# Optimization experiments

Hardware: AMD Instinct MI355X
Metric: run time of the kernel (lower is better)

The kernel has to match this reference:

```python
import jax, jax.numpy as jnp
import numpy as np

EMBED_DIM = 1024
N_HEAD = 16

def setup_inputs() -> dict:
    key = jax.random.key(0)
    ks = jax.random.split(key, 5)
    C = EMBED_DIM
    x = jax.random.normal(ks[0], (2, 2048, C), dtype=jnp.float32)
    s = 1.0 / np.sqrt(C)
    W_attn = jax.random.normal(ks[1], (C, 3 * C), dtype=jnp.float32) * s
    b_attn = jnp.zeros((3 * C,), dtype=jnp.float32)
    W_proj = jax.random.normal(ks[2], (C, C), dtype=jnp.float32) * s
    b_proj = jnp.zeros((C,), dtype=jnp.float32)
    return {"x": x, "W_attn": W_attn, "b_attn": b_attn, "W_proj": W_proj, "b_proj": b_proj}

def reference(x, W_attn, b_attn, W_proj, b_proj):
    B, T, C = x.shape
    H = N_HEAD
    D = C // H
    qkv = x @ W_attn + b_attn                      # [B,T,3C]
    q, k, v = jnp.split(qkv, 3, axis=-1)
    # [B,H,T,D]
    q = q.reshape(B, T, H, D).transpose(0, 2, 1, 3)
    k = k.reshape(B, T, H, D).transpose(0, 2, 1, 3)
    v = v.reshape(B, T, H, D).transpose(0, 2, 1, 3)
    att = jnp.einsum('bhqd,bhkd->bhqk', q, k) * (1.0 / jnp.sqrt(jnp.asarray(D, x.dtype)))
    causal = jnp.tril(jnp.ones((T, T), dtype=bool))
    att = jnp.where(causal, att, -jnp.inf)
    att = jax.nn.softmax(att, axis=-1)
    y = jnp.einsum('bhqk,bhkd->bhqd', att, v)      # [B,H,T,D]
    y = y.transpose(0, 2, 1, 3).reshape(B, T, C)
    return y @ W_proj + b_proj
```

## Files before the change

### kernel.cpp

```cpp
#include <hip/hip_runtime.h>
#include <stdint.h>

typedef __attribute__((ext_vector_type(4))) float f32x4;
typedef __attribute__((ext_vector_type(8))) __bf16 bf16x8;
typedef __attribute__((ext_vector_type(8))) unsigned short u16x8;

__device__ __forceinline__ unsigned short f2b(float f) {
  unsigned u = __float_as_uint(f);
  u += 0x7FFFu + ((u >> 16) & 1u);
  return (unsigned short)(u >> 16);
}
__device__ __forceinline__ float b2f(unsigned short s) {
  unsigned u = (unsigned)s << 16;
  return __uint_as_float(u);
}
__device__ __forceinline__ unsigned cvtpk_bf16(float lo, float hi) {
  unsigned r;
  asm("v_cvt_pk_bf16_f32 %0, %1, %2" : "=v"(r) : "v"(lo), "v"(hi));
  return r;
}

__device__ __forceinline__ void gload_lds16(const void* g, void* l) {
  typedef __attribute__((address_space(1))) void GV1;
  typedef __attribute__((address_space(3))) void LV3;
  __builtin_amdgcn_global_load_lds((GV1*)(void*)g, (LV3*)l, 16, 0, 0);
}

__device__ __forceinline__ void tile_barrier_keep2() {
  asm volatile("s_waitcnt vmcnt(2)" ::: "memory");
  __builtin_amdgcn_sched_barrier(0);
  __builtin_amdgcn_s_barrier();
  __builtin_amdgcn_sched_barrier(0);
}
__device__ __forceinline__ void tile_barrier_keep0() {
  asm volatile("s_waitcnt vmcnt(0)" ::: "memory");
  __builtin_amdgcn_sched_barrier(0);
  __builtin_amdgcn_s_barrier();
  __builtin_amdgcn_sched_barrier(0);
}

__global__ __launch_bounds__(256) void convert_f32_bf16(const float* __restrict__ in,
                                                        unsigned short* __restrict__ out, int n) {
  int i = (blockIdx.x * 256 + threadIdx.x) * 8;
  if (i >= n) return;
  float4 a = *(const float4*)(in + i);
  float4 b = *(const float4*)(in + i + 4);
  u16x8 r;
  r[0] = f2b(a.x); r[1] = f2b(a.y); r[2] = f2b(a.z); r[3] = f2b(a.w);
  r[4] = f2b(b.x); r[5] = f2b(b.y); r[6] = f2b(b.z); r[7] = f2b(b.w);
  *(u16x8*)(out + i) = r;
}

__global__ __launch_bounds__(256) void transpose_f32_bf16(const float* __restrict__ W,
                                                          unsigned short* __restrict__ Wt,
                                                          int K, int N) {
  __shared__ unsigned short tile[32][33];
  int n0 = blockIdx.x * 32, k0 = blockIdx.y * 32;
  int tx = threadIdx.x, ty = threadIdx.y;
  #pragma unroll
  for (int j = 0; j < 32; j += 8)
    tile[ty + j][tx] = f2b(W[(size_t)(k0 + ty + j) * N + n0 + tx]);
  __syncthreads();
  #pragma unroll
  for (int j = 0; j < 32; j += 8)
    Wt[(size_t)(n0 + ty + j) * K + k0 + tx] = tile[tx][ty + j];
}

template <bool OUT_BF16, bool VSPLIT>
__global__ __launch_bounds__(512) void gemm_bt(const unsigned short* __restrict__ A,
                                               const unsigned short* __restrict__ Bt,
                                               const float* __restrict__ bias,
                                               void* __restrict__ Cout,
                                               unsigned short* __restrict__ vT,
                                               int M, int N, int K) {
  __shared__ unsigned short SMEM[32768];
  const int m0 = blockIdx.x * 128, n0 = blockIdx.y * 128;
  const int tid = threadIdx.x;
  const int w = tid >> 6, l = tid & 63;
  const int wm = w >> 2, wn = w & 3;
  const int c = l & 15, g = l >> 4;
  const int NT = K >> 6;
  const unsigned short* aptr[2];
  const unsigned short* bptr[2];
  #pragma unroll
  for (int i = 0; i < 2; ++i) {
    int rb = w * 16 + i * 8;
    aptr[i] = A  + (size_t)(m0 + rb + (l >> 3)) * K + (l & 7) * 8;
    bptr[i] = Bt + (size_t)(n0 + rb + (l >> 3)) * K + (l & 7) * 8;
  }
  f32x4 acc[4][2] = {};
  #pragma unroll
  for (int i = 0; i < 2; ++i) {
    int rb = w * 16 + i * 8;
    gload_lds16(aptr[i], &SMEM[rb * 64]);
    gload_lds16(bptr[i], &SMEM[8192 + rb * 64]);
  }
  __syncthreads();
  for (int t = 0; t < NT; ++t) {
    const int cur = t & 1;
    const unsigned short* Ab = &SMEM[cur * 16384];
    const unsigned short* Bb = &SMEM[cur * 16384 + 8192];
    if (t + 1 < NT) {
      unsigned short* An = &SMEM[(cur ^ 1) * 16384];
      unsigned short* Bn = &SMEM[(cur ^ 1) * 16384 + 8192];
      #pragma unroll
      for (int i = 0; i < 2; ++i) {
        int rb = w * 16 + i * 8;
        gload_lds16(aptr[i] + (size_t)(t + 1) * 64, &An[rb * 64]);
        gload_lds16(bptr[i] + (size_t)(t + 1) * 64, &Bn[rb * 64]);
      }
    }
    #pragma unroll
    for (int ks = 0; ks < 2; ++ks) {
      bf16x8 af[4], bf[2];
      #pragma unroll
      for (int mi = 0; mi < 4; ++mi)
        af[mi] = *(const bf16x8*)&Ab[(wm * 64 + mi * 16 + c) * 64 + ks * 32 + g * 8];
      #pragma unroll
      for (int ni = 0; ni < 2; ++ni)
        bf[ni] = *(const bf16x8*)&Bb[(wn * 32 + ni * 16 + c) * 64 + ks * 32 + g * 8];
      __builtin_amdgcn_s_setprio(1);
      #pragma unroll
      for (int mi = 0; mi < 4; ++mi)
        #pragma unroll
        for (int ni = 0; ni < 2; ++ni)
          acc[mi][ni] = __builtin_amdgcn_mfma_f32_16x16x32_bf16(af[mi], bf[ni], acc[mi][ni], 0, 0, 0);
      __builtin_amdgcn_s_setprio(0);
    }
    __syncthreads();
  }
  if (VSPLIT && n0 >= 2048) {
    unsigned short* TR = SMEM;
    #pragma unroll
    for (int mi = 0; mi < 4; ++mi)
      #pragma unroll
      for (int ni = 0; ni < 2; ++ni) {
        int cl = wn * 32 + ni * 16 + c;
        float bv = bias[n0 + cl];
        int rlb = wm * 64 + mi * 16 + 4 * g;
        ushort4 o4;
        o4.x = f2b(acc[mi][ni][0] + bv); o4.y = f2b(acc[mi][ni][1] + bv);
        o4.z = f2b(acc[mi][ni][2] + bv); o4.w = f2b(acc[mi][ni][3] + bv);
        *(ushort4*)&TR[cl * 136 + rlb] = o4;
      }
    __syncthreads();
    const int d0 = n0 - 2048;
    #pragma unroll
    for (int p = 0; p < 4; ++p) {
      int rowl = p * 32 + (tid >> 4);
      *(u16x8*)(vT + (size_t)(d0 + rowl) * 4096 + m0 + (tid & 15) * 8) =
          *(const u16x8*)&TR[rowl * 136 + (tid & 15) * 8];
    }
    return;
  }
  const int NS = VSPLIT ? 2048 : N;
  #pragma unroll
  for (int mi = 0; mi < 4; ++mi) {
    #pragma unroll
    for (int ni = 0; ni < 2; ++ni) {
      int colg = n0 + wn * 32 + ni * 16 + c;
      float bv = bias[colg];
      #pragma unroll
      for (int r = 0; r < 4; ++r) {
        int rowg = m0 + wm * 64 + mi * 16 + 4 * g + r;
        float v = acc[mi][ni][r] + bv;
        if (OUT_BF16)
          ((unsigned short*)Cout)[(size_t)rowg * NS + colg] = f2b(v);
        else
          ((float*)Cout)[(size_t)rowg * NS + colg] = v;
      }
    }
  }
}

__global__ __launch_bounds__(512) void attn_kernel(const unsigned short* __restrict__ qk,
                                                   const unsigned short* __restrict__ vT,
                                                   unsigned short* __restrict__ partO,
                                                   float* __restrict__ partML) {
  __shared__ unsigned short K_lds[3][64 * 64];
  __shared__ unsigned short V_lds[3][64 * 64];
  const int bid = blockIdx.x;
  const int bh = bid & 31;
  const int cid = 39 - (bid >> 5);
  int qt, ct;
  if (cid < 4)       { qt = cid;            ct = 0; }
  else if (cid < 12) { int e = cid - 4;  qt = 4 + (e >> 1);  ct = e & 1; }
  else if (cid < 24) { int e = cid - 12; int q3 = e / 3; qt = 8 + q3; ct = e - 3 * q3; }
  else               { int e = cid - 24; qt = 12 + (e >> 2); ct = e & 3; }
  const int ntt = 2 * qt + 2;
  const int t0 = ct * 8;
  const int ntl = min(ntt - t0, 8);
  const int b = bh >> 4, h = bh & 15;
  const int tid = threadIdx.x, w = tid >> 6, l = tid & 63;
  const int c = l & 15, g = l >> 4;
  const int hi = g >> 1;
  const int srcA = c + ((g & 1) << 5);
  const int srcB = srcA + 16;
  const size_t row0 = (size_t)b * 2048;
  const float SCL = 0.18033688f;
  const int KSTRIDE = 64 * 2048;
  const int VSTRIDE = 64;

  const int q0w = qt * 128 + w * 16;
  const int qg = q0w + c;

  bf16x8 qf[2];
  #pragma unroll
  for (int ks = 0; ks < 2; ++ks)
    qf[ks] = *(const bf16x8*)(qk + (row0 + qg) * 2048 + h * 64 + ks * 32 + g * 8);

  f32x4 acc[4] = {};
  float mstate = -1e30f, lstate = 0.f;

  const int krow = w * 8 + (l >> 3);
  const int kch = (l & 7) ^ (krow & 7);
  const unsigned short* kptr = qk + (row0 + t0 * 64 + krow) * 2048 + 1024 + h * 64 + kch * 8;
  const unsigned short* vptr = vT + (size_t)(h * 64 + krow) * 4096 + (b * 2048 + t0 * 64) + kch * 8;
  const int kdst = (w * 8) * 64;

  gload_lds16(kptr, &K_lds[0][kdst]);
  gload_lds16(vptr, &V_lds[0][kdst]);
  if (ntl > 1) {
    gload_lds16(kptr + KSTRIDE, &K_lds[1][kdst]);
    gload_lds16(vptr + VSTRIDE, &V_lds[1][kdst]);
    tile_barrier_keep2();
  } else {
    tile_barrier_keep0();
  }

  int cur = 0;
  for (int lt = 0; lt < ntl; ++lt) {
    const int kv0 = (t0 + lt) * 64;
    const bool pre2 = (lt + 2 < ntl);
    if (pre2) {
      int sb = cur + 2; if (sb >= 3) sb -= 3;
      gload_lds16(kptr + 2 * KSTRIDE, &K_lds[sb][kdst]);
      gload_lds16(vptr + 2 * VSTRIDE, &V_lds[sb][kdst]);
    }
    kptr += KSTRIDE;
    vptr += VSTRIDE;
    if (kv0 <= q0w + 15) {
      const char* Kb = (const char*)K_lds[cur];
      const char* Vb = (const char*)V_lds[cur];
      f32x4 s[4] = {};
      #pragma unroll
      for (int ks = 0; ks < 2; ++ks) {
        bf16x8 kf[4];
        #pragma unroll
        for (int nk = 0; nk < 4; ++nk) {
          int row = nk * 16 + c;
          kf[nk] = *(const bf16x8*)(Kb + row * 128 + ((ks * 64 + g * 16) ^ ((row & 7) << 4)));
        }
        __builtin_amdgcn_s_setprio(1);
        #pragma unroll
        for (int nk = 0; nk < 4; ++nk)
          s[nk] = __builtin_amdgcn_mfma_f32_16x16x32_bf16(kf[nk], qf[ks], s[nk], 0, 0, 0);
        __builtin_amdgcn_s_setprio(0);
      }
      if (kv0 + 63 > q0w) {
        #pragma unroll
        for (int nk = 0; nk < 4; ++nk)
          #pragma unroll
          for (int r = 0; r < 4; ++r) {
            int kvg = kv0 + nk * 16 + 4 * g + r;
            if (kvg > qg) s[nk][r] = -1e30f;
          }
      }
      float a0 = fmaxf(fmaxf(s[0][0], s[0][1]), fmaxf(s[0][2], s[0][3]));
      float a1 = fmaxf(fmaxf(s[1][0], s[1][1]), fmaxf(s[1][2], s[1][3]));
      float a2 = fmaxf(fmaxf(s[2][0], s[2][1]), fmaxf(s[2][2], s[2][3]));
      float a3 = fmaxf(fmaxf(s[3][0], s[3][1]), fmaxf(s[3][2], s[3][3]));
      float mx = fmaxf(fmaxf(a0, a1), fmaxf(a2, a3));
      mx = fmaxf(mx, __shfl_xor(mx, 16));
      mx = fmaxf(mx, __shfl_xor(mx, 32));
      if (!__all(mx <= mstate)) {
        float mnew = fmaxf(mstate, mx);
        float alpha = exp2f((mstate - mnew) * SCL);
        mstate = mnew;
        lstate *= alpha;
        #pragma unroll
        for (int nd = 0; nd < 4; ++nd) acc[nd] *= alpha;
      }
      float ms = mstate * SCL;
      #pragma unroll
      for (int nk = 0; nk < 4; ++nk) {
        #pragma unroll
        for (int r = 0; r < 4; ++r) s[nk][r] = exp2f(fmaf(s[nk][r], SCL, -ms));
        lstate += (s[nk][0] + s[nk][1]) + (s[nk][2] + s[nk][3]);
      }
      unsigned pk[4][2];
      #pragma unroll
      for (int nk = 0; nk < 4; ++nk) {
        pk[nk][0] = cvtpk_bf16(s[nk][0], s[nk][1]);
        pk[nk][1] = cvtpk_bf16(s[nk][2], s[nk][3]);
      }
      #pragma unroll
      for (int vks = 0; vks < 2; ++vks) {
        unsigned rA00 = __shfl(pk[2 * vks][0], srcA, 64);
        unsigned rA01 = __shfl(pk[2 * vks][1], srcA, 64);
        unsigned rA10 = __shfl(pk[2 * vks + 1][0], srcA, 64);
        unsigned rA11 = __shfl(pk[2 * vks + 1][1], srcA, 64);
        unsigned rB00 = __shfl(pk[2 * vks][0], srcB, 64);
        unsigned rB01 = __shfl(pk[2 * vks][1], srcB, 64);
        unsigned rB10 = __shfl(pk[2 * vks + 1][0], srcB, 64);
        unsigned rB11 = __shfl(pk[2 * vks + 1][1], srcB, 64);
        union { unsigned u[4]; bf16x8 v; } pa;
        pa.u[0] = hi ? rA10 : rA00;
        pa.u[1] = hi ? rA11 : rA01;
        pa.u[2] = hi ? rB10 : rB00;
        pa.u[3] = hi ? rB11 : rB01;
        bf16x8 vf[4];
        #pragma unroll
        for (int nd = 0; nd < 4; ++nd) {
          int row = nd * 16 + c;
          vf[nd] = *(const bf16x8*)(Vb + row * 128 + ((vks * 64 + g * 16) ^ ((row & 7) << 4)));
        }
        __builtin_amdgcn_s_setprio(1);
        #pragma unroll
        for (int nd = 0; nd < 4; ++nd)
          acc[nd] = __builtin_amdgcn_mfma_f32_16x16x32_bf16(vf[nd], pa.v, acc[nd], 0, 0, 0);
        __builtin_amdgcn_s_setprio(0);
      }
    }
    if (lt + 1 < ntl) {
      if (pre2) tile_barrier_keep2();
      else      tile_barrier_keep0();
    }
    cur = (cur + 1 == 3) ? 0 : cur + 1;
  }

  float lsum = lstate;
  lsum += __shfl_xor(lsum, 16);
  lsum += __shfl_xor(lsum, 32);
  const int qrow = w * 16 + c;
  #pragma unroll
  for (int nd = 0; nd < 4; ++nd) {
    ushort4 o4;
    o4.x = f2b(acc[nd][0]); o4.y = f2b(acc[nd][1]);
    o4.z = f2b(acc[nd][2]); o4.w = f2b(acc[nd][3]);
    *(ushort4*)(partO + (size_t)bid * 8192 + qrow * 64 + nd * 16 + 4 * g) = o4;
  }
  if (g == 0) {
    partML[(size_t)bid * 256 + qrow * 2 + 0] = mstate;
    partML[(size_t)bid * 256 + qrow * 2 + 1] = lsum;
  }
}

__global__ __launch_bounds__(256) void attn_combine(const unsigned short* __restrict__ partO,
                                                    const float* __restrict__ partML,
                                                    unsigned short* __restrict__ out) {
  const int bid = blockIdx.x;
  const int qt = bid >> 5, bh = bid & 31;
  const int b = bh >> 4, h = bh & 15;
  const int np = (2 * qt + 9) >> 3;
  const int base = (qt < 4) ? qt
                 : (qt < 8) ? 4 + 2 * (qt - 4)
                 : (qt < 12) ? 12 + 3 * (qt - 8)
                 : 24 + 4 * (qt - 12);
  const int t = threadIdx.x;
  const int row = t >> 1, cg = (t & 1) * 32;
  const float SCL = 0.18033688f;
  float mstar = -1e30f;
  #pragma unroll
  for (int p = 0; p < 4; ++p)
    if (p < np)
      mstar = fmaxf(mstar, partML[(size_t)(((39 - (base + p)) << 5) | bh) * 256 + row * 2]);
  float L = 0.f;
  float o[32];
  #pragma unroll
  for (int j = 0; j < 32; ++j) o[j] = 0.f;
  #pragma unroll
  for (int p = 0; p < 4; ++p) {
    if (p < np) {
      int slot = ((39 - (base + p)) << 5) | bh;
      float mp = partML[(size_t)slot * 256 + row * 2 + 0];
      float lp = partML[(size_t)slot * 256 + row * 2 + 1];
      float wgt = exp2f((mp - mstar) * SCL);
      L = fmaf(wgt, lp, L);
      const unsigned short* src = partO + (size_t)slot * 8192 + row * 64 + cg;
      #pragma unroll
      for (int q = 0; q < 4; ++q) {
        u16x8 a = *(const u16x8*)(src + q * 8);
        #pragma unroll
        for (int j = 0; j < 8; ++j)
          o[q * 8 + j] = fmaf(b2f(a[j]), wgt, o[q * 8 + j]);
      }
    }
  }
  float rinv = 1.0f / L;
  size_t trow = (size_t)b * 2048 + qt * 128 + row;
  #pragma unroll
  for (int q = 0; q < 4; ++q) {
    u16x8 r;
    #pragma unroll
    for (int j = 0; j < 8; ++j) r[j] = f2b(o[q * 8 + j] * rinv);
    *(u16x8*)(out + trow * 1024 + h * 64 + cg + q * 8) = r;
  }
}

extern "C" void kernel_launch(void* const* d_in, const int* in_sizes, int n_in,
                              void* d_out, int out_size, void* d_ws, size_t ws_size,
                              hipStream_t stream) {
  const float* x      = (const float*)d_in[0];
  const float* W_attn = (const float*)d_in[1];
  const float* b_attn = (const float*)d_in[2];
  const float* W_proj = (const float*)d_in[3];
  const float* b_proj = (const float*)d_in[4];
  float* out = (float*)d_out;

  char* ws = (char*)d_ws;
  unsigned short* Wproj_t  = (unsigned short*)(ws + 0);
  unsigned short* qk       = (unsigned short*)(ws + 2097152);
  unsigned short* vT       = (unsigned short*)(ws + 18874368);
  unsigned short* x_bf     = (unsigned short*)(ws + 27262976);
  unsigned short* Wattn_t  = (unsigned short*)(ws + 35651584);
  unsigned short* partO    = (unsigned short*)(ws + 27262976);
  unsigned short* attn_out = (unsigned short*)(ws + 48234496);
  float*          partML   = (float*)(ws + 56623104);

  convert_f32_bf16<<<2048, 256, 0, stream>>>(x, x_bf, 4194304);
  transpose_f32_bf16<<<dim3(96, 32), dim3(32, 8), 0, stream>>>(W_attn, Wattn_t, 1024, 3072);
  transpose_f32_bf16<<<dim3(32, 32), dim3(32, 8), 0, stream>>>(W_proj, Wproj_t, 1024, 1024);

  gemm_bt<true, true><<<dim3(32, 24), 512, 0, stream>>>(x_bf, Wattn_t, b_attn, qk, vT,
                                                        4096, 3072, 1024);
  attn_kernel<<<1280, 512, 0, stream>>>(qk, vT, partO, partML);
  attn_combine<<<512, 256, 0, stream>>>(partO, partML, attn_out);
  gemm_bt<false, false><<<dim3(32, 8), 512, 0, stream>>>(attn_out, Wproj_t, b_proj, out, nullptr,
                                                         4096, 1024, 1024);
}
```

Baseline: 137.9 us.

## Restructure GEMM to 4 waves with triple-buffered 32-wide K tiles

The GEMM kernel drops from 8 waves of 512 threads to 4 waves of 256 threads. Each wave now computes a 64x64 sub-tile with 16 accumulators instead of 8. The K step shrinks from 64 to 32 and loads are triple-buffered with two tiles prefetched ahead, using partial vmcnt waits before each barrier, so more memory latency is hidden. This costs more accumulator registers per thread, more barriers per K, and fewer waves per block to hide latency. The V-transpose epilogue is adjusted to the new thread count.

```diff
diff --git a/kernel.cpp b/kernel.cpp
--- a/kernel.cpp
+++ b/kernel.cpp
@@ -26,6 +26,12 @@
   __builtin_amdgcn_global_load_lds((GV1*)(void*)g, (LV3*)l, 16, 0, 0);
 }
 
+__device__ __forceinline__ void tile_barrier_keep4() {
+  asm volatile("s_waitcnt vmcnt(4)" ::: "memory");
+  __builtin_amdgcn_sched_barrier(0);
+  __builtin_amdgcn_s_barrier();
+  __builtin_amdgcn_sched_barrier(0);
+}
 __device__ __forceinline__ void tile_barrier_keep2() {
   asm volatile("s_waitcnt vmcnt(2)" ::: "memory");
   __builtin_amdgcn_sched_barrier(0);
@@ -67,75 +73,87 @@
 }
 
 template <bool OUT_BF16, bool VSPLIT>
-__global__ __launch_bounds__(512) void gemm_bt(const unsigned short* __restrict__ A,
+__global__ __launch_bounds__(256) void gemm_bt(const unsigned short* __restrict__ A,
                                                const unsigned short* __restrict__ Bt,
                                                const float* __restrict__ bias,
                                                void* __restrict__ Cout,
                                                unsigned short* __restrict__ vT,
                                                int M, int N, int K) {
-  __shared__ unsigned short SMEM[32768];
+  __shared__ unsigned short SMEM[24576];
   const int m0 = blockIdx.x * 128, n0 = blockIdx.y * 128;
   const int tid = threadIdx.x;
   const int w = tid >> 6, l = tid & 63;
-  const int wm = w >> 2, wn = w & 3;
+  const int wm = w >> 1, wn = w & 1;
   const int c = l & 15, g = l >> 4;
-  const int NT = K >> 6;
+  const int NT = K >> 5;
   const unsigned short* aptr[2];
   const unsigned short* bptr[2];
   #pragma unroll
   for (int i = 0; i < 2; ++i) {
-    int rb = w * 16 + i * 8;
-    aptr[i] = A  + (size_t)(m0 + rb + (l >> 3)) * K + (l & 7) * 8;
-    bptr[i] = Bt + (size_t)(n0 + rb + (l >> 3)) * K + (l & 7) * 8;
-  }
-  f32x4 acc[4][2] = {};
+    int rb = w * 32 + i * 16;
+    aptr[i] = A  + (size_t)(m0 + rb + (l >> 2)) * K + (l & 3) * 8;
+    bptr[i] = Bt + (size_t)(n0 + rb + (l >> 2)) * K + (l & 3) * 8;
+  }
+  f32x4 acc[4][4] = {};
   #pragma unroll
   for (int i = 0; i < 2; ++i) {
-    int rb = w * 16 + i * 8;
-    gload_lds16(aptr[i], &SMEM[rb * 64]);
-    gload_lds16(bptr[i], &SMEM[8192 + rb * 64]);
-  }
-  __syncthreads();
+    int rb = w * 32 + i * 16;
+    gload_lds16(aptr[i], &SMEM[rb * 32]);
+    gload_lds16(bptr[i], &SMEM[4096 + rb * 32]);
+  }
+  if (NT > 1) {
+    #pragma unroll
+    for (int i = 0; i < 2; ++i) {
+      int rb = w * 32 + i * 16;
+      gload_lds16(aptr[i] + 32, &SMEM[8192 + rb * 32]);
+      gload_lds16(bptr[i] + 32, &SMEM[8192 + 4096 + rb * 32]);
+    }
+    tile_barrier_keep4();
+  } else {
+    tile_barrier_keep0();
+  }
+  int cur = 0;
   for (int t = 0; t < NT; ++t) {
-    const int cur = t & 1;
-    const unsigned short* Ab = &SMEM[cur * 16384];
-    const unsigned short* Bb = &SMEM[cur * 16384 + 8192];
+    const bool pre2 = (t + 2 < NT);
+    if (pre2) {
+      int sb = cur + 2; if (sb >= 3) sb -= 3;
+      #pragma unroll
+      for (int i = 0; i < 2; ++i) {
+        int rb = w * 32 + i * 16;
+        gload_lds16(aptr[i] + (size_t)(t + 2) * 32, &SMEM[sb * 8192 + rb * 32]);
+        gload_lds16(bptr[i] + (size_t)(t + 2) * 32, &SMEM[sb * 8192 + 4096 + rb * 32]);
+      }
+    }
+    const unsigned short* Ab = &SMEM[cur * 8192];
+    const unsigned short* Bb = &SMEM[cur * 8192 + 4096];
+    bf16x8 af[4], bf[4];
+    #pragma unroll
+    for (int mi = 0; mi < 4; ++mi)
+      af[mi] = *(const bf16x8*)&Ab[(wm * 64 + mi * 16 + c) * 32 + g * 8];
+    #pragma unroll
+    for (int ni = 0; ni < 4; ++ni)
+      bf[ni] = *(const bf16x8*)&Bb[(wn * 64 + ni * 16 + c) * 32 + g * 8];
+    __builtin_amdgcn_s_setprio(1);
+    #pragma unroll
+    for (int mi = 0; mi < 4; ++mi)
+      #pragma unroll
+      for (int ni = 0; ni < 4; ++ni)
+        acc[mi][ni] = __builtin_amdgcn_mfma_f32_16x16x32_bf16(af[mi], bf[ni], acc[mi][ni], 0, 0, 0);
+    __builtin_amdgcn_s_setprio(0);
     if (t + 1 < NT) {
-      unsigned short* An = &SMEM[(cur ^ 1) * 16384];
-      unsigned short* Bn = &SMEM[(cur ^ 1) * 16384 + 8192];
-      #pragma unroll
-      for (int i = 0; i < 2; ++i) {
-        int rb = w * 16 + i * 8;
-        gload_lds16(aptr[i] + (size_t)(t + 1) * 64, &An[rb * 64]);
-        gload_lds16(bptr[i] + (size_t)(t + 1) * 64, &Bn[rb * 64]);
-      }
-    }
-    #pragma unroll
-    for (int ks = 0; ks < 2; ++ks) {
-      bf16x8 af[4], bf[2];
-      #pragma unroll
-      for (int mi = 0; mi < 4; ++mi)
-        af[mi] = *(const bf16x8*)&Ab[(wm * 64 + mi * 16 + c) * 64 + ks * 32 + g * 8];
-      #pragma unroll
-      for (int ni = 0; ni < 2; ++ni)
-        bf[ni] = *(const bf16x8*)&Bb[(wn * 32 + ni * 16 + c) * 64 + ks * 32 + g * 8];
-      __builtin_amdgcn_s_setprio(1);
-      #pragma unroll
-      for (int mi = 0; mi < 4; ++mi)
-        #pragma unroll
-        for (int ni = 0; ni < 2; ++ni)
-          acc[mi][ni] = __builtin_amdgcn_mfma_f32_16x16x32_bf16(af[mi], bf[ni], acc[mi][ni], 0, 0, 0);
-      __builtin_amdgcn_s_setprio(0);
-    }
+      if (pre2) tile_barrier_keep4();
+      else      tile_barrier_keep0();
+    }
+    cur = (cur + 1 == 3) ? 0 : cur + 1;
+  }
+  if (VSPLIT && n0 >= 2048) {
     __syncthreads();
-  }
-  if (VSPLIT && n0 >= 2048) {
     unsigned short* TR = SMEM;
     #pragma unroll
     for (int mi = 0; mi < 4; ++mi)
       #pragma unroll
-      for (int ni = 0; ni < 2; ++ni) {
-        int cl = wn * 32 + ni * 16 + c;
+      for (int ni = 0; ni < 4; ++ni) {
+        int cl = wn * 64 + ni * 16 + c;
         float bv = bias[n0 + cl];
         int rlb = wm * 64 + mi * 16 + 4 * g;
         ushort4 o4;
@@ -146,8 +164,8 @@
     __syncthreads();
     const int d0 = n0 - 2048;
     #pragma unroll
-    for (int p = 0; p < 4; ++p) {
-      int rowl = p * 32 + (tid >> 4);
+    for (int p = 0; p < 8; ++p) {
+      int rowl = p * 16 + (tid >> 4);
       *(u16x8*)(vT + (size_t)(d0 + rowl) * 4096 + m0 + (tid & 15) * 8) =
           *(const u16x8*)&TR[rowl * 136 + (tid & 15) * 8];
     }
@@ -157,8 +175,8 @@
   #pragma unroll
   for (int mi = 0; mi < 4; ++mi) {
     #pragma unroll
-    for (int ni = 0; ni < 2; ++ni) {
-      int colg = n0 + wn * 32 + ni * 16 + c;
+    for (int ni = 0; ni < 4; ++ni) {
+      int colg = n0 + wn * 64 + ni * 16 + c;
       float bv = bias[colg];
       #pragma unroll
       for (int r = 0; r < 4; ++r) {
@@ -422,10 +440,10 @@
   transpose_f32_bf16<<<dim3(96, 32), dim3(32, 8), 0, stream>>>(W_attn, Wattn_t, 1024, 3072);
   transpose_f32_bf16<<<dim3(32, 32), dim3(32, 8), 0, stream>>>(W_proj, Wproj_t, 1024, 1024);
 
-  gemm_bt<true, true><<<dim3(32, 24), 512, 0, stream>>>(x_bf, Wattn_t, b_attn, qk, vT,
+  gemm_bt<true, true><<<dim3(32, 24), 256, 0, stream>>>(x_bf, Wattn_t, b_attn, qk, vT,
                                                         4096, 3072, 1024);
   attn_kernel<<<1280, 512, 0, stream>>>(qk, vT, partO, partML);
   attn_combine<<<512, 256, 0, stream>>>(partO, partML, attn_out);
-  gemm_bt<false, false><<<dim3(32, 8), 512, 0, stream>>>(attn_out, Wproj_t, b_proj, out, nullptr,
+  gemm_bt<false, false><<<dim3(32, 8), 256, 0, stream>>>(attn_out, Wproj_t, b_proj, out, nullptr,
                                                          4096, 1024, 1024);
 }
```

After: 134.8 us (median of 3 runs). -2.2%, faster.
